# Kernel optimization log

Measured on AMD Instinct MI355X. Metric: run time of the kernel, lower is better.

The kernel has to match this reference:

```python
import math
import jax, jax.numpy as jnp
import numpy as np

# dims: batch, in-channels, out-channels, features (freq bins), frames, heads, expansion
B, C, CO, F, W, NH, EXP = 1, 8, 8, 512, 256, 8, 4
CC = C + CO          # channels into cross-attn query (cat of h and self_attn)
FC = C + 2 * CO      # channels into FFN (cat of h, self_attn, src_attn)
FH = F * EXP         # FFN hidden features


def mc_linear(x, pw, dw=None):
    # x: [B,Cin,Fin,W]; pw: [Cin,Fout,Fin] per-channel positionwise matmul;
    # dw: [Cout,Cin] channel-mixing matmul ('depthwise' in the repo's naming)
    y = jnp.einsum('bcfw,cgf->bcgw', x, pw)
    if dw is not None:
        y = jnp.einsum('bcgw,oc->bogw', y, dw)
    return y


def frame_conv(x, w, b):
    # Conv2d kernel (1,3), padding (0,1): 1D conv along the frame axis
    y = jax.lax.conv_general_dilated(x, w, (1, 1), ((0, 0), (1, 1)),
                                     dimension_numbers=('NCHW', 'OIHW', 'NCHW'))
    return y + b[None, :, None, None]


def mc_layernorm(x, g, b, eps=1e-5):
    # normalize over the feature axis (2), per (batch, channel, frame)
    mu = x.mean(axis=2, keepdims=True)
    var = jnp.mean(jnp.square(x - mu), axis=2, keepdims=True)
    return (x - mu) * jax.lax.rsqrt(var + eps) * g[None, :, :, None] + b[None, :, :, None]


def mc_attention(xq, xkv, q_pw, q_dw, q_cw, q_cb, k_pw, k_cw, k_cb, v_pw, v_cw, v_cb, o_pw):
    q = frame_conv(mc_linear(xq, q_pw, q_dw), q_cw, q_cb)   # [B,CO,F,Wq]
    k = frame_conv(mc_linear(xkv, k_pw), k_cw, k_cb)        # [B,CO,F,Wk]
    v = frame_conv(mc_linear(xkv, v_pw), v_cw, v_cb)
    dh = F // NH

    def heads(t):  # [B,CO,F,Wt] -> [B,CO,NH,Wt,dh]
        b_, c_, f_, w_ = t.shape
        return t.transpose(0, 1, 3, 2).reshape(b_, c_, w_, NH, dh).transpose(0, 1, 3, 2, 4)

    qh, kh, vh = heads(q), heads(k), heads(v)
    qk = jnp.einsum('bchqd,bchkd->bchqk', qh, kh) / math.sqrt(F)
    a = jnp.einsum('bchqk,bchkd->bchqd', jax.nn.softmax(qk, axis=-1), vh)
    b_, c_, h_, w_, _ = a.shape
    a = a.transpose(0, 1, 3, 2, 4).reshape(b_, c_, w_, F).transpose(0, 1, 3, 2)  # [B,CO,F,Wq]
    return mc_linear(a, o_pw), qk


def setup_inputs() -> dict:
    key = jax.random.key(0)
    ks = jax.random.split(key, 32)
    it = iter(range(32))

    def rn(shape, s=0.02):
        return jax.random.normal(ks[next(it)], shape, jnp.float32) * s

    inp = {
        'x': jax.random.normal(ks[next(it)], (B, C, F, W), jnp.float32),
        'src': jax.random.normal(ks[next(it)], (B, C, F, W), jnp.float32),
        'ln_g': jnp.ones((C, F), jnp.float32),
        'ln_b': jnp.zeros((C, F), jnp.float32),
        # self-attention (C -> CO, C == CO so no channel-mix on projections)
        'sa_q_pw': rn((C, F, F)), 'sa_q_cw': rn((CO, CO, 1, 3), 0.1), 'sa_q_cb': jnp.zeros((CO,), jnp.float32),
        'sa_k_pw': rn((C, F, F)), 'sa_k_cw': rn((CO, CO, 1, 3), 0.1), 'sa_k_cb': jnp.zeros((CO,), jnp.float32),
        'sa_v_pw': rn((C, F, F)), 'sa_v_cw': rn((CO, CO, 1, 3), 0.1), 'sa_v_cb': jnp.zeros((CO,), jnp.float32),
        'sa_o_pw': rn((CO, F, F)),
        # cross-attention (query from CC=C+CO channels -> CO; key/value from src with C channels)
        'ca_q_pw': rn((CC, F, F)), 'ca_q_dw': rn((CO, CC), 0.1),
        'ca_q_cw': rn((CO, CO, 1, 3), 0.1), 'ca_q_cb': jnp.zeros((CO,), jnp.float32),
        'ca_k_pw': rn((C, F, F)), 'ca_k_cw': rn((CO, CO, 1, 3), 0.1), 'ca_k_cb': jnp.zeros((CO,), jnp.float32),
        'ca_v_pw': rn((C, F, F)), 'ca_v_cw': rn((CO, CO, 1, 3), 0.1), 'ca_v_cb': jnp.zeros((CO,), jnp.float32),
        'ca_o_pw': rn((CO, F, F)),
        # FFN
        'ffn1_pw': rn((FC, FH, F)), 'ffn1_dw': rn((FC, FC), 0.1),
        'ffn2_pw': rn((FC, F, FH)), 'ffn2_dw': rn((C, FC), 0.1),
    }
    return inp


def reference(x, src, ln_g, ln_b,
              sa_q_pw, sa_q_cw, sa_q_cb, sa_k_pw, sa_k_cw, sa_k_cb, sa_v_pw, sa_v_cw, sa_v_cb, sa_o_pw,
              ca_q_pw, ca_q_dw, ca_q_cw, ca_q_cb, ca_k_pw, ca_k_cw, ca_k_cb, ca_v_pw, ca_v_cw, ca_v_cb, ca_o_pw,
              ffn1_pw, ffn1_dw, ffn2_pw, ffn2_dw):
    h = mc_layernorm(x, ln_g, ln_b)
    sa, qk1 = mc_attention(h, h, sa_q_pw, None, sa_q_cw, sa_q_cb,
                           sa_k_pw, sa_k_cw, sa_k_cb, sa_v_pw, sa_v_cw, sa_v_cb, sa_o_pw)
    ca, qk2 = mc_attention(jnp.concatenate([h, sa], axis=1), src,
                           ca_q_pw, ca_q_dw, ca_q_cw, ca_q_cb,
                           ca_k_pw, ca_k_cw, ca_k_cb, ca_v_pw, ca_v_cw, ca_v_cb, ca_o_pw)
    z = mc_linear(jnp.concatenate([h, sa, ca], axis=1), ffn1_pw, ffn1_dw)
    z = jax.nn.gelu(z, approximate=False)
    z = mc_linear(z, ffn2_pw, ffn2_dw)
    return (x + z, qk1, qk2)
```

## Files before the change

kernel.cpp:

```cpp
#include <hip/hip_runtime.h>
#include <math.h>

typedef __attribute__((ext_vector_type(4))) float f32x4;
typedef __attribute__((ext_vector_type(8))) short s16x8;
typedef __attribute__((ext_vector_type(4))) short s16x4;

__device__ __forceinline__ unsigned short f2b(float f) {
    union { float f; unsigned u; } v; v.f = f;
    unsigned r = v.u + 0x7fffu + ((v.u >> 16) & 1u);
    return (unsigned short)(r >> 16);
}
__device__ __forceinline__ float b2f(unsigned short u) {
    union { unsigned u; float f; } v; v.u = ((unsigned)u) << 16;
    return v.f;
}

__device__ __forceinline__ void gll16(const void* g, void* l) {
    __builtin_amdgcn_global_load_lds((const __attribute__((address_space(1))) unsigned int*)g,
                                     (__attribute__((address_space(3))) unsigned int*)l,
                                     16, 0, 0);
}

constexpr int kF = 512;
constexpr int kW = 256;
constexpr int kFW = kF * kW;

__global__ __launch_bounds__(256) void prep_kernel(const float* __restrict__ x,
                                                   const float* __restrict__ g,
                                                   const float* __restrict__ b,
                                                   unsigned short* __restrict__ hTb,
                                                   const float* __restrict__ src,
                                                   unsigned short* __restrict__ SRCT) {
    __shared__ float tile[64][65];
    __shared__ float s1[16][16], s2[16][16];
    int bid = blockIdx.x;
    int t = threadIdx.x;
    if (bid < 128) {
        int c = bid >> 4;
        int w0 = (bid & 15) * 16;
        int wi = t & 15, fg = t >> 4;
        const float* xb = x + (size_t)c * kFW + w0 + wi;
        float sum = 0.f, sum2 = 0.f;
        for (int j = 0; j < 32; ++j) {
            float v = xb[(size_t)(fg * 32 + j) * kW];
            sum += v; sum2 += v * v;
        }
        s1[fg][wi] = sum; s2[fg][wi] = sum2;
        __syncthreads();
        float ts = 0.f, tq = 0.f;
        #pragma unroll
        for (int j = 0; j < 16; ++j) { ts += s1[j][wi]; tq += s2[j][wi]; }
        float mu = ts * (1.0f / 512.0f);
        float rstd = rsqrtf(tq * (1.0f / 512.0f) - mu * mu + 1e-5f);
        const float* gc = g + c * kF + fg * 32;
        const float* bc = b + c * kF + fg * 32;
        unsigned short* ob = hTb + (size_t)c * kFW + (size_t)(w0 + wi) * kF + fg * 32;
        for (int j = 0; j < 32; j += 4) {
            float v0 = xb[(size_t)(fg * 32 + j + 0) * kW];
            float v1 = xb[(size_t)(fg * 32 + j + 1) * kW];
            float v2 = xb[(size_t)(fg * 32 + j + 2) * kW];
            float v3 = xb[(size_t)(fg * 32 + j + 3) * kW];
            s16x4 p = { (short)f2b((v0 - mu) * rstd * gc[j + 0] + bc[j + 0]),
                        (short)f2b((v1 - mu) * rstd * gc[j + 1] + bc[j + 1]),
                        (short)f2b((v2 - mu) * rstd * gc[j + 2] + bc[j + 2]),
                        (short)f2b((v3 - mu) * rstd * gc[j + 3] + bc[j + 3]) };
            *(s16x4*)(&ob[j]) = p;
        }
    } else {
        int fid = bid - 128;
        int c = fid >> 5;
        int f0 = ((fid >> 2) & 7) * 64, w0 = (fid & 3) * 64;
        int tw = t & 63, tf4 = t >> 6;
        for (int i = 0; i < 16; ++i) {
            int f = tf4 * 16 + i;
            tile[f][tw] = src[(size_t)c * kFW + (size_t)(f0 + f) * kW + w0 + tw];
        }
        __syncthreads();
        int w = t >> 2, fc = (t & 3) * 16;
        unsigned short* ob = SRCT + (size_t)c * kFW + (size_t)(w0 + w) * kF + f0 + fc;
        for (int j = 0; j < 16; j += 4) {
            s16x4 p = { (short)f2b(tile[fc + j + 0][w]), (short)f2b(tile[fc + j + 1][w]),
                        (short)f2b(tile[fc + j + 2][w]), (short)f2b(tile[fc + j + 3][w]) };
            *(s16x4*)(&ob[j]) = p;
        }
    }
}

struct WSeg { const float* A; const unsigned short* B; void* C; int omode; };
struct WB8 { WSeg s[8]; };

__global__ __launch_bounds__(256) void wgemm256(WB8 wb, int M, int K, int Klocal,
                                                long a_ch, long b_ch, long c_ch, long c_split,
                                                int segshift, int nm, int ksplit) {
    __shared__ unsigned short lds[16384];
    int t = threadIdx.x, lane = t & 63, wv = t >> 6;
    int l16 = lane & 15, l4 = lane >> 4;

    int id = blockIdx.x;
    int r = id & 7, j = id >> 3;
    int per = nm * ksplit;
    int y = r + 8 * (j / per);
    int rem = j % per;
    int mt = rem % nm;
    int kz = rem / nm;
    int seg = y >> segshift, c = y & ((1 << segshift) - 1);
    WSeg sg = wb.s[seg];
    int bm = mt * 64;
    int kbase = kz * Klocal;

    const float* A = sg.A + (size_t)c * a_ch + kbase;
    const unsigned short* Bc = sg.B + (size_t)c * b_ch + kbase;
    const float* arow = A + (size_t)(bm + wv * 16 + l16) * K + l4 * 8;

    int rsub = lane >> 3;
    int gsw = ((lane & 7) ^ rsub) * 8;
    const unsigned short* bsrc = Bc + (size_t)rsub * K + gsw;

    f32x4 acc[16];
    #pragma unroll
    for (int i = 0; i < 16; ++i) acc[i] = (f32x4){0.f, 0.f, 0.f, 0.f};

    f32x4 pa0 = __builtin_nontemporal_load((const f32x4*)arow);
    f32x4 pa1 = __builtin_nontemporal_load((const f32x4*)(arow + 4));

    for (int kc = 0; kc < Klocal; kc += 64) {
        if (kc) __syncthreads();
        #pragma unroll
        for (int i = 0; i < 8; ++i) {
            int r0 = wv * 64 + i * 8;
            gll16(bsrc + (size_t)r0 * K + kc, (char*)lds + (r0 << 7));
        }
        __syncthreads();
        #pragma unroll
        for (int ks = 0; ks < 2; ++ks) {
            f32x4 c0 = pa0, c1 = pa1;
            int nk = kc + (ks + 1) * 32;
            if (nk < Klocal) {
                pa0 = __builtin_nontemporal_load((const f32x4*)(arow + nk));
                pa1 = __builtin_nontemporal_load((const f32x4*)(arow + nk + 4));
            }
            s16x8 af = { (short)f2b(c0.x), (short)f2b(c0.y), (short)f2b(c0.z), (short)f2b(c0.w),
                         (short)f2b(c1.x), (short)f2b(c1.y), (short)f2b(c1.z), (short)f2b(c1.w) };
            #pragma unroll
            for (int ni = 0; ni < 16; ++ni) {
                int rr = ni * 16 + l16;
                s16x8 bf = *(const s16x8*)(&lds[rr * 64 + ((ks * 32 + l4 * 8) ^ ((rr & 7) << 3))]);
                acc[ni] = __builtin_amdgcn_mfma_f32_16x16x32_bf16(af, bf, acc[ni], 0, 0, 0);
            }
        }
    }

    int m0 = bm + wv * 16 + l4 * 4;
    if (sg.omode == 2) {
        unsigned short* C = (unsigned short*)sg.C + (size_t)c * c_ch;
        #pragma unroll
        for (int ni = 0; ni < 16; ++ni) {
            int n = ni * 16 + l16;
            s16x4 pk = { (short)f2b(acc[ni][0]), (short)f2b(acc[ni][1]),
                         (short)f2b(acc[ni][2]), (short)f2b(acc[ni][3]) };
            *(s16x4*)(&C[(size_t)n * M + m0]) = pk;
        }
    } else if (sg.omode == 1) {
        unsigned short* C = (unsigned short*)sg.C + (size_t)c * c_ch;
        #pragma unroll
        for (int ni = 0; ni < 16; ++ni) {
            int n = ni * 16 + l16;
            #pragma unroll
            for (int rr = 0; rr < 4; ++rr)
                C[(size_t)(m0 + rr) * 256 + n] = f2b(acc[ni][rr]);
        }
    } else {
        float* C = (float*)sg.C + (size_t)c * c_ch + (size_t)kz * c_split;
        #pragma unroll
        for (int ni = 0; ni < 16; ++ni) {
            int n = ni * 16 + l16;
            #pragma unroll
            for (int rr = 0; rr < 4; ++rr)
                C[(size_t)(m0 + rr) * 256 + n] = acc[ni][rr];
        }
    }
}

__global__ __launch_bounds__(256) void attn_kernel(
    const unsigned short* __restrict__ Qt, const unsigned short* __restrict__ Kt,
    const unsigned short* __restrict__ VN, float* __restrict__ S,
    unsigned short* __restrict__ ATTT, float scale)
{
    __shared__ unsigned short q_lds[4096];
    __shared__ unsigned short kv_lds[16384];
    __shared__ unsigned short p_lds[16384];
    __shared__ float smax[4][64], ssum[4][64], sinv[64];
    int t = threadIdx.x, lane = t & 63, wv = t >> 6;
    int l16 = lane & 15, l4 = lane >> 4;
    int ch = blockIdx.y, c = ch >> 3, h = ch & 7;
    int bm = blockIdx.x * 64;
    const unsigned short* Qb = Qt + (size_t)c * kFW + h * 64;
    const unsigned short* Kb = Kt + (size_t)c * kFW + h * 64;
    const unsigned short* Vb = VN + (size_t)c * kFW + (size_t)(h * 64) * 256;
    float* Sb = S + (size_t)ch * 65536;
    unsigned short* Ab = ATTT + (size_t)c * kFW + h * 64;

    s16x8 qr[2], kr[8], vr[8];
    #pragma unroll
    for (int i = 0; i < 2; ++i) {
        int idx = i * 256 + t; int rr = idx >> 3, ck = idx & 7;
        qr[i] = *(const s16x8*)(Qb + (size_t)(bm + rr) * 512 + ck * 8);
    }
    #pragma unroll
    for (int i = 0; i < 8; ++i) {
        int idx = i * 256 + t; int rr = idx >> 3, ck = idx & 7;
        kr[i] = *(const s16x8*)(Kb + (size_t)rr * 512 + ck * 8);
    }
    #pragma unroll
    for (int i = 0; i < 8; ++i) {
        int idx = i * 256 + t; int d = idx >> 5, cs = idx & 31;
        vr[i] = *(const s16x8*)(Vb + (size_t)d * 256 + cs * 8);
    }
    #pragma unroll
    for (int i = 0; i < 2; ++i) {
        int idx = i * 256 + t; int rr = idx >> 3, ck = idx & 7;
        *(s16x8*)(&q_lds[rr * 64 + ((ck * 8) ^ ((rr & 7) << 3))]) = qr[i];
    }
    #pragma unroll
    for (int i = 0; i < 8; ++i) {
        int idx = i * 256 + t; int rr = idx >> 3, ck = idx & 7;
        *(s16x8*)(&kv_lds[rr * 64 + ((ck * 8) ^ ((rr & 7) << 3))]) = kr[i];
    }
    __syncthreads();

    f32x4 acc[4][4];
    #pragma unroll
    for (int i = 0; i < 4; ++i)
        #pragma unroll
        for (int jj = 0; jj < 4; ++jj) acc[i][jj] = (f32x4){0.f, 0.f, 0.f, 0.f};
    #pragma unroll
    for (int ks = 0; ks < 2; ++ks) {
        s16x8 af[4], bfr[4];
        #pragma unroll
        for (int mi = 0; mi < 4; ++mi) {
            int rq = mi * 16 + l16;
            af[mi] = *(const s16x8*)(&q_lds[rq * 64 + ((ks * 32 + l4 * 8) ^ ((rq & 7) << 3))]);
        }
        #pragma unroll
        for (int ni = 0; ni < 4; ++ni) {
            int rk = wv * 64 + ni * 16 + l16;
            bfr[ni] = *(const s16x8*)(&kv_lds[rk * 64 + ((ks * 32 + l4 * 8) ^ ((rk & 7) << 3))]);
        }
        #pragma unroll
        for (int mi = 0; mi < 4; ++mi)
            #pragma unroll
            for (int ni = 0; ni < 4; ++ni)
                acc[mi][ni] = __builtin_amdgcn_mfma_f32_16x16x32_bf16(af[mi], bfr[ni], acc[mi][ni], 0, 0, 0);
    }

    #pragma unroll
    for (int mi = 0; mi < 4; ++mi)
        #pragma unroll
        for (int ni = 0; ni < 4; ++ni) {
            acc[mi][ni] *= scale;
            int col = wv * 64 + ni * 16 + l16;
            int row0 = bm + mi * 16 + l4 * 4;
            #pragma unroll
            for (int rr = 0; rr < 4; ++rr)
                Sb[(size_t)(row0 + rr) * 256 + col] = acc[mi][ni][rr];
        }

    float rmax[4][4];
    #pragma unroll
    for (int mi = 0; mi < 4; ++mi)
        #pragma unroll
        for (int rr = 0; rr < 4; ++rr)
            rmax[mi][rr] = fmaxf(fmaxf(acc[mi][0][rr], acc[mi][1][rr]), fmaxf(acc[mi][2][rr], acc[mi][3][rr]));
    #pragma unroll
    for (int d = 1; d < 16; d <<= 1)
        #pragma unroll
        for (int mi = 0; mi < 4; ++mi)
            #pragma unroll
            for (int rr = 0; rr < 4; ++rr)
                rmax[mi][rr] = fmaxf(rmax[mi][rr], __shfl_xor(rmax[mi][rr], d));
    if (l16 == 0)
        #pragma unroll
        for (int mi = 0; mi < 4; ++mi)
            #pragma unroll
            for (int rr = 0; rr < 4; ++rr)
                smax[wv][mi * 16 + l4 * 4 + rr] = rmax[mi][rr];
    __syncthreads();
    float rsum[4][4];
    #pragma unroll
    for (int mi = 0; mi < 4; ++mi)
        #pragma unroll
        for (int rr = 0; rr < 4; ++rr) {
            int row = mi * 16 + l4 * 4 + rr;
            float rM = fmaxf(fmaxf(smax[0][row], smax[1][row]), fmaxf(smax[2][row], smax[3][row]));
            rsum[mi][rr] = 0.f;
            #pragma unroll
            for (int ni = 0; ni < 4; ++ni) {
                float e = __expf(acc[mi][ni][rr] - rM);
                acc[mi][ni][rr] = e;
                rsum[mi][rr] += e;
            }
        }
    #pragma unroll
    for (int d = 1; d < 16; d <<= 1)
        #pragma unroll
        for (int mi = 0; mi < 4; ++mi)
            #pragma unroll
            for (int rr = 0; rr < 4; ++rr)
                rsum[mi][rr] += __shfl_xor(rsum[mi][rr], d);
    if (l16 == 0)
        #pragma unroll
        for (int mi = 0; mi < 4; ++mi)
            #pragma unroll
            for (int rr = 0; rr < 4; ++rr)
                ssum[wv][mi * 16 + l4 * 4 + rr] = rsum[mi][rr];
    __syncthreads();

    #pragma unroll
    for (int i = 0; i < 8; ++i) {
        int idx = i * 256 + t; int d = idx >> 5, cs = idx & 31;
        *(s16x8*)(&kv_lds[d * 256 + ((cs * 8) ^ ((d & 7) << 3))]) = vr[i];
    }
    #pragma unroll
    for (int mi = 0; mi < 4; ++mi)
        #pragma unroll
        for (int ni = 0; ni < 4; ++ni) {
            int col = wv * 64 + ni * 16 + l16;
            int cb = col & ~7, cl = col & 7;
            #pragma unroll
            for (int rr = 0; rr < 4; ++rr) {
                int row = mi * 16 + l4 * 4 + rr;
                p_lds[row * 256 + (cb ^ ((row & 7) << 3)) + cl] = f2b(acc[mi][ni][rr]);
            }
        }
    if (t < 64) sinv[t] = 1.f / (ssum[0][t] + ssum[1][t] + ssum[2][t] + ssum[3][t]);
    __syncthreads();

    f32x4 po[4];
    #pragma unroll
    for (int ni = 0; ni < 4; ++ni) po[ni] = (f32x4){0.f, 0.f, 0.f, 0.f};
    int qrow = wv * 16 + l16;
    #pragma unroll
    for (int ks = 0; ks < 8; ++ks) {
        s16x8 paf = *(const s16x8*)(&p_lds[qrow * 256 + ((ks * 32 + l4 * 8) ^ ((qrow & 7) << 3))]);
        #pragma unroll
        for (int ni = 0; ni < 4; ++ni) {
            int rd = ni * 16 + l16;
            s16x8 bf = *(const s16x8*)(&kv_lds[rd * 256 + ((ks * 32 + l4 * 8) ^ ((rd & 7) << 3))]);
            po[ni] = __builtin_amdgcn_mfma_f32_16x16x32_bf16(paf, bf, po[ni], 0, 0, 0);
        }
    }
    #pragma unroll
    for (int ni = 0; ni < 4; ++ni) {
        int d = ni * 16 + l16;
        #pragma unroll
        for (int rr = 0; rr < 4; ++rr) {
            int row = wv * 16 + l4 * 4 + rr;
            Ab[(size_t)(bm + row) * 512 + d] = f2b(po[ni][rr] * sinv[row]);
        }
    }
}

struct ConvArgs {
    const unsigned short* in[5];
    unsigned short* out[5];
    const float* cw[5];
    const float* cb[5];
    int mode[5];
};

__global__ __launch_bounds__(256) void conv5_kernel(ConvArgs a) {
    int g = blockIdx.y;
    __shared__ float scw[192]; __shared__ float scb[8];
    int t = threadIdx.x;
    if (t < 192) scw[t] = a.cw[g][t];
    if (t >= 192 && t < 200) scb[t - 192] = a.cb[g][t - 192];
    __syncthreads();
    const unsigned short* in = a.in[g];
    unsigned short* out = a.out[g];
    int gi = blockIdx.x * 256 + t;
    int mode = a.mode[g];
    int w = mode ? (gi & 255) : (gi >> 9);
    int str = mode ? 1 : 512;
    float acc[8];
    #pragma unroll
    for (int o = 0; o < 8; ++o) acc[o] = scb[o];
    bool hm = w > 0, hp = w < 255;
    #pragma unroll
    for (int i = 0; i < 8; ++i) {
        size_t base = (size_t)i * kFW + gi;
        float xm = hm ? b2f(in[base - str]) : 0.f;
        float x0 = b2f(in[base]);
        float xp = hp ? b2f(in[base + str]) : 0.f;
        #pragma unroll
        for (int o = 0; o < 8; ++o) {
            const float* wp = &scw[(o * 8 + i) * 3];
            acc[o] += wp[0] * xm + wp[1] * x0 + wp[2] * xp;
        }
    }
    #pragma unroll
    for (int o = 0; o < 8; ++o) out[(size_t)o * kFW + gi] = f2b(acc[o]);
}

__global__ __launch_bounds__(256) void mixconv_kernel(const unsigned short* __restrict__ in,
                                                      const float* __restrict__ dw,
                                                      const float* __restrict__ cw,
                                                      const float* __restrict__ cb,
                                                      unsigned short* __restrict__ out) {
    __shared__ float sdw[128], scw[192], scb[8];
    int t = threadIdx.x;
    if (t < 128) sdw[t] = dw[t];
    if (t >= 128 && t < 136) scb[t - 128] = cb[t - 128];
    if (t < 192) scw[t] = cw[t];
    __syncthreads();
    int gi = blockIdx.x * 256 + t;
    int w = gi >> 9;
    bool hm = w > 0, hp = w < 255;
    float xc[16], xm[16], xp[16];
    #pragma unroll
    for (int cc = 0; cc < 16; ++cc) {
        size_t base = (size_t)cc * kFW + gi;
        xc[cc] = b2f(in[base]);
        xm[cc] = hm ? b2f(in[base - 512]) : 0.f;
        xp[cc] = hp ? b2f(in[base + 512]) : 0.f;
    }
    float mm[8], m0[8], mp[8];
    #pragma unroll
    for (int o = 0; o < 8; ++o) {
        float am = 0.f, a0 = 0.f, ap = 0.f;
        #pragma unroll
        for (int cc = 0; cc < 16; ++cc) {
            float wv = sdw[o * 16 + cc];
            am += wv * xm[cc]; a0 += wv * xc[cc]; ap += wv * xp[cc];
        }
        mm[o] = am; m0[o] = a0; mp[o] = ap;
    }
    #pragma unroll
    for (int o = 0; o < 8; ++o) {
        float acc = scb[o];
        #pragma unroll
        for (int i = 0; i < 8; ++i) {
            const float* wp = &scw[(o * 8 + i) * 3];
            acc += wp[0] * mm[i] + wp[1] * m0[i] + wp[2] * mp[i];
        }
        out[(size_t)o * kFW + gi] = f2b(acc);
    }
}

__global__ __launch_bounds__(256) void gelu24_kernel(unsigned short* __restrict__ z,
                                                     const float* __restrict__ dw) {
    __shared__ float sdw[576];
    int t = threadIdx.x;
    for (int i = t; i < 576; i += 256) sdw[i] = dw[i];
    __syncthreads();
    size_t gi = (size_t)blockIdx.x * 256 + t;
    const size_t CH = (size_t)256 * 2048;
    float xv[24];
    #pragma unroll
    for (int cc = 0; cc < 24; ++cc) xv[cc] = b2f(z[cc * CH + gi]);
    #pragma unroll
    for (int o = 0; o < 24; ++o) {
        float s = 0.f;
        #pragma unroll
        for (int cc = 0; cc < 24; ++cc) s += sdw[o * 24 + cc] * xv[cc];
        s = 0.5f * s * (1.0f + erff(s * 0.7071067811865475f));
        z[o * CH + gi] = f2b(s);
    }
}

__global__ __launch_bounds__(256) void final_mix_add2(const float* __restrict__ x,
                                                      const float* __restrict__ z2,
                                                      const float* __restrict__ dw,
                                                      float* __restrict__ out) {
    __shared__ float sdw[192];
    int t = threadIdx.x;
    if (t < 192) sdw[t] = dw[t];
    __syncthreads();
    int gi = blockIdx.x * 256 + t;
    const size_t PSZ = (size_t)24 * kFW;
    float xv[24];
    #pragma unroll
    for (int cc = 0; cc < 24; ++cc) {
        size_t o = (size_t)cc * kFW + gi;
        xv[cc] = z2[o] + z2[PSZ + o];
    }
    #pragma unroll
    for (int o = 0; o < 8; ++o) {
        float s = 0.f;
        #pragma unroll
        for (int cc = 0; cc < 24; ++cc) s += sdw[o * 24 + cc] * xv[cc];
        out[(size_t)o * kFW + gi] = x[(size_t)o * kFW + gi] + s;
    }
}

extern "C" void kernel_launch(void* const* d_in, const int* in_sizes, int n_in,
                              void* d_out, int out_size, void* d_ws, size_t ws_size,
                              hipStream_t stream) {
    const float* x       = (const float*)d_in[0];
    const float* src     = (const float*)d_in[1];
    const float* ln_g    = (const float*)d_in[2];
    const float* ln_b    = (const float*)d_in[3];
    const float* sa_q_pw = (const float*)d_in[4];
    const float* sa_q_cw = (const float*)d_in[5];
    const float* sa_q_cb = (const float*)d_in[6];
    const float* sa_k_pw = (const float*)d_in[7];
    const float* sa_k_cw = (const float*)d_in[8];
    const float* sa_k_cb = (const float*)d_in[9];
    const float* sa_v_pw = (const float*)d_in[10];
    const float* sa_v_cw = (const float*)d_in[11];
    const float* sa_v_cb = (const float*)d_in[12];
    const float* sa_o_pw = (const float*)d_in[13];
    const float* ca_q_pw = (const float*)d_in[14];
    const float* ca_q_dw = (const float*)d_in[15];
    const float* ca_q_cw = (const float*)d_in[16];
    const float* ca_q_cb = (const float*)d_in[17];
    const float* ca_k_pw = (const float*)d_in[18];
    const float* ca_k_cw = (const float*)d_in[19];
    const float* ca_k_cb = (const float*)d_in[20];
    const float* ca_v_pw = (const float*)d_in[21];
    const float* ca_v_cw = (const float*)d_in[22];
    const float* ca_v_cb = (const float*)d_in[23];
    const float* ca_o_pw = (const float*)d_in[24];
    const float* ffn1_pw = (const float*)d_in[25];
    const float* ffn1_dw = (const float*)d_in[26];
    const float* ffn2_pw = (const float*)d_in[27];
    const float* ffn2_dw = (const float*)d_in[28];

    float* out  = (float*)d_out;
    float* qk1o = out + 1048576;
    float* qk2o = out + 1048576 + 4194304;

    unsigned char* ws = (unsigned char*)d_ws;
    unsigned short* CAT24  = (unsigned short*)(ws + 0);
    unsigned short* hTb    = CAT24;
    unsigned short* saTb   = CAT24 + 8 * (size_t)kFW;
    unsigned short* caTb   = CAT24 + 16 * (size_t)kFW;
    unsigned short* SRCT   = (unsigned short*)(ws + 6291456);
    unsigned short* preQ   = (unsigned short*)(ws + 8388608);
    unsigned short* preK   = (unsigned short*)(ws + 10485760);
    unsigned short* preVsa = (unsigned short*)(ws + 12582912);
    unsigned short* preKca = (unsigned short*)(ws + 14680064);
    unsigned short* preVca = (unsigned short*)(ws + 16777216);
    unsigned short* QT     = (unsigned short*)(ws + 18874368);
    unsigned short* KT     = (unsigned short*)(ws + 20971520);
    unsigned short* VNsa   = (unsigned short*)(ws + 23068672);
    unsigned short* KTca   = (unsigned short*)(ws + 25165824);
    unsigned short* VNca   = (unsigned short*)(ws + 27262976);
    unsigned short* PRE16  = (unsigned short*)(ws + 29360128);
    unsigned short* QTca   = (unsigned short*)(ws + 33554432);
    unsigned short* ATTT   = (unsigned short*)(ws + 35651584);
    unsigned short* Z0T    = (unsigned short*)(ws + 8388608);
    float*          Z2P    = (float*)(ws + 37748736);

    const float qscale = 0.044194173824159216f;
    dim3 blk(256);

    prep_kernel<<<384, blk, 0, stream>>>(x, ln_g, ln_b, hTb, src, SRCT);

    WB8 p6;
    p6.s[0] = { sa_q_pw, hTb,  preQ,   2 };
    p6.s[1] = { sa_k_pw, hTb,  preK,   2 };
    p6.s[2] = { sa_v_pw, hTb,  preVsa, 1 };
    p6.s[3] = { ca_k_pw, SRCT, preKca, 2 };
    p6.s[4] = { ca_v_pw, SRCT, preVca, 1 };
    p6.s[5] = { ca_q_pw, hTb,  PRE16,  2 };
    p6.s[6] = p6.s[0]; p6.s[7] = p6.s[0];
    wgemm256<<<dim3(384), blk, 0, stream>>>(p6, 512, 512, 512, 262144, kFW, kFW, 0, 3, 8, 1);

    ConvArgs c5;
    c5.in[0] = preQ;   c5.out[0] = QT;   c5.cw[0] = sa_q_cw; c5.cb[0] = sa_q_cb; c5.mode[0] = 0;
    c5.in[1] = preK;   c5.out[1] = KT;   c5.cw[1] = sa_k_cw; c5.cb[1] = sa_k_cb; c5.mode[1] = 0;
    c5.in[2] = preVsa; c5.out[2] = VNsa; c5.cw[2] = sa_v_cw; c5.cb[2] = sa_v_cb; c5.mode[2] = 1;
    c5.in[3] = preKca; c5.out[3] = KTca; c5.cw[3] = ca_k_cw; c5.cb[3] = ca_k_cb; c5.mode[3] = 0;
    c5.in[4] = preVca; c5.out[4] = VNca; c5.cw[4] = ca_v_cw; c5.cb[4] = ca_v_cb; c5.mode[4] = 1;
    conv5_kernel<<<dim3(512, 5), blk, 0, stream>>>(c5);

    attn_kernel<<<dim3(4, 64), blk, 0, stream>>>(QT, KT, VNsa, qk1o, ATTT, qscale);
    WB8 so;
    so.s[0] = { sa_o_pw, ATTT, saTb, 2 };
    for (int i = 1; i < 8; ++i) so.s[i] = so.s[0];
    wgemm256<<<dim3(64), blk, 0, stream>>>(so, 512, 512, 512, 262144, kFW, kFW, 0, 8, 8, 1);

    WB8 cq2;
    cq2.s[0] = { ca_q_pw + 8 * 262144, saTb, PRE16 + 8 * (size_t)kFW, 2 };
    for (int i = 1; i < 8; ++i) cq2.s[i] = cq2.s[0];
    wgemm256<<<dim3(64), blk, 0, stream>>>(cq2, 512, 512, 512, 262144, kFW, kFW, 0, 8, 8, 1);
    mixconv_kernel<<<512, blk, 0, stream>>>(PRE16, ca_q_dw, ca_q_cw, ca_q_cb, QTca);

    attn_kernel<<<dim3(4, 64), blk, 0, stream>>>(QTca, KTca, VNca, qk2o, ATTT, qscale);
    WB8 co;
    co.s[0] = { ca_o_pw, ATTT, caTb, 2 };
    for (int i = 1; i < 8; ++i) co.s[i] = co.s[0];
    wgemm256<<<dim3(64), blk, 0, stream>>>(co, 512, 512, 512, 262144, kFW, kFW, 0, 8, 8, 1);

    WB8 f1;
    f1.s[0] = { ffn1_pw, CAT24, Z0T, 2 };
    for (int i = 1; i < 8; ++i) f1.s[i] = f1.s[0];
    wgemm256<<<dim3(768), blk, 0, stream>>>(f1, 2048, 512, 512, 1048576, kFW, 524288, 0, 8, 32, 1);
    gelu24_kernel<<<2048, blk, 0, stream>>>(Z0T, ffn1_dw);
    WB8 f2;
    f2.s[0] = { ffn2_pw, Z0T, Z2P, 0 };
    for (int i = 1; i < 8; ++i) f2.s[i] = f2.s[0];
    wgemm256<<<dim3(384), blk, 0, stream>>>(f2, 512, 2048, 1024, 1048576, 524288, kFW, 3145728, 8, 8, 2);
    final_mix_add2<<<512, blk, 0, stream>>>(x, Z2P, ffn2_dw, out);
}
```

Baseline: 271.7 us.

## Use 512-thread GEMM blocks with 128-row tiles and double-buffered B in LDS

The batched per-channel GEMM now runs 8 waves per block covering 128 output rows, so each B tile staged in LDS is shared by twice as many rows. B loads are double-buffered, with the next 64-wide K chunk prefetched while MFMAs run on the current one, which removes one barrier per iteration. Grid sizes are halved to match. The cost is twice the LDS per block (64 KB) and fewer blocks, which may reduce occupancy and leave CUs idle on the small 32-block launches.

```diff
diff --git a/kernel.cpp b/kernel.cpp
--- a/kernel.cpp
+++ b/kernel.cpp
@@ -89,10 +89,10 @@
 struct WSeg { const float* A; const unsigned short* B; void* C; int omode; };
 struct WB8 { WSeg s[8]; };
 
-__global__ __launch_bounds__(256) void wgemm256(WB8 wb, int M, int K, int Klocal,
+__global__ __launch_bounds__(512) void wgemm512(WB8 wb, int M, int K, int Klocal,
                                                 long a_ch, long b_ch, long c_ch, long c_split,
                                                 int segshift, int nm, int ksplit) {
-    __shared__ unsigned short lds[16384];
+    __shared__ unsigned short lds[2][16384];
     int t = threadIdx.x, lane = t & 63, wv = t >> 6;
     int l16 = lane & 15, l4 = lane >> 4;
 
@@ -105,7 +105,7 @@
     int kz = rem / nm;
     int seg = y >> segshift, c = y & ((1 << segshift) - 1);
     WSeg sg = wb.s[seg];
-    int bm = mt * 64;
+    int bm = mt * 128;
     int kbase = kz * Klocal;
 
     const float* A = sg.A + (size_t)c * a_ch + kbase;
@@ -114,27 +114,34 @@
 
     int rsub = lane >> 3;
     int gsw = ((lane & 7) ^ rsub) * 8;
-    const unsigned short* bsrc = Bc + (size_t)rsub * K + gsw;
+    const unsigned short* bsrc = Bc + (size_t)(wv * 32 + rsub) * K + gsw;
 
     f32x4 acc[16];
     #pragma unroll
     for (int i = 0; i < 16; ++i) acc[i] = (f32x4){0.f, 0.f, 0.f, 0.f};
+
+    #pragma unroll
+    for (int i = 0; i < 4; ++i)
+        gll16(bsrc + (size_t)(i * 8) * K, (char*)lds[0] + ((wv * 32 + i * 8) << 7));
 
     f32x4 pa0 = __builtin_nontemporal_load((const f32x4*)arow);
     f32x4 pa1 = __builtin_nontemporal_load((const f32x4*)(arow + 4));
 
-    for (int kc = 0; kc < Klocal; kc += 64) {
-        if (kc) __syncthreads();
-        #pragma unroll
-        for (int i = 0; i < 8; ++i) {
-            int r0 = wv * 64 + i * 8;
-            gll16(bsrc + (size_t)r0 * K + kc, (char*)lds + (r0 << 7));
-        }
+    int nc = Klocal >> 6;
+    for (int cc = 0; cc < nc; ++cc) {
         __syncthreads();
+        if (cc + 1 < nc) {
+            int kc = (cc + 1) * 64;
+            #pragma unroll
+            for (int i = 0; i < 4; ++i)
+                gll16(bsrc + (size_t)(i * 8) * K + kc,
+                      (char*)lds[(cc + 1) & 1] + ((wv * 32 + i * 8) << 7));
+        }
+        const unsigned short* buf = lds[cc & 1];
         #pragma unroll
         for (int ks = 0; ks < 2; ++ks) {
             f32x4 c0 = pa0, c1 = pa1;
-            int nk = kc + (ks + 1) * 32;
+            int nk = cc * 64 + (ks + 1) * 32;
             if (nk < Klocal) {
                 pa0 = __builtin_nontemporal_load((const f32x4*)(arow + nk));
                 pa1 = __builtin_nontemporal_load((const f32x4*)(arow + nk + 4));
@@ -144,7 +151,7 @@
             #pragma unroll
             for (int ni = 0; ni < 16; ++ni) {
                 int rr = ni * 16 + l16;
-                s16x8 bf = *(const s16x8*)(&lds[rr * 64 + ((ks * 32 + l4 * 8) ^ ((rr & 7) << 3))]);
+                s16x8 bf = *(const s16x8*)(&buf[rr * 64 + ((ks * 32 + l4 * 8) ^ ((rr & 7) << 3))]);
                 acc[ni] = __builtin_amdgcn_mfma_f32_16x16x32_bf16(af, bf, acc[ni], 0, 0, 0);
             }
         }
@@ -553,6 +560,7 @@
 
     const float qscale = 0.044194173824159216f;
     dim3 blk(256);
+    dim3 blk512(512);
 
     prep_kernel<<<384, blk, 0, stream>>>(x, ln_g, ln_b, hTb, src, SRCT);
 
@@ -564,7 +572,7 @@
     p6.s[4] = { ca_v_pw, SRCT, preVca, 1 };
     p6.s[5] = { ca_q_pw, hTb,  PRE16,  2 };
     p6.s[6] = p6.s[0]; p6.s[7] = p6.s[0];
-    wgemm256<<<dim3(384), blk, 0, stream>>>(p6, 512, 512, 512, 262144, kFW, kFW, 0, 3, 8, 1);
+    wgemm512<<<dim3(192), blk512, 0, stream>>>(p6, 512, 512, 512, 262144, kFW, kFW, 0, 3, 4, 1);
 
     ConvArgs c5;
     c5.in[0] = preQ;   c5.out[0] = QT;   c5.cw[0] = sa_q_cw; c5.cb[0] = sa_q_cb; c5.mode[0] = 0;
@@ -578,28 +586,28 @@
     WB8 so;
     so.s[0] = { sa_o_pw, ATTT, saTb, 2 };
     for (int i = 1; i < 8; ++i) so.s[i] = so.s[0];
-    wgemm256<<<dim3(64), blk, 0, stream>>>(so, 512, 512, 512, 262144, kFW, kFW, 0, 8, 8, 1);
+    wgemm512<<<dim3(32), blk512, 0, stream>>>(so, 512, 512, 512, 262144, kFW, kFW, 0, 8, 4, 1);
 
     WB8 cq2;
     cq2.s[0] = { ca_q_pw + 8 * 262144, saTb, PRE16 + 8 * (size_t)kFW, 2 };
     for (int i = 1; i < 8; ++i) cq2.s[i] = cq2.s[0];
-    wgemm256<<<dim3(64), blk, 0, stream>>>(cq2, 512, 512, 512, 262144, kFW, kFW, 0, 8, 8, 1);
+    wgemm512<<<dim3(32), blk512, 0, stream>>>(cq2, 512, 512, 512, 262144, kFW, kFW, 0, 8, 4, 1);
     mixconv_kernel<<<512, blk, 0, stream>>>(PRE16, ca_q_dw, ca_q_cw, ca_q_cb, QTca);
 
     attn_kernel<<<dim3(4, 64), blk, 0, stream>>>(QTca, KTca, VNca, qk2o, ATTT, qscale);
     WB8 co;
     co.s[0] = { ca_o_pw, ATTT, caTb, 2 };
     for (int i = 1; i < 8; ++i) co.s[i] = co.s[0];
-    wgemm256<<<dim3(64), blk, 0, stream>>>(co, 512, 512, 512, 262144, kFW, kFW, 0, 8, 8, 1);
+    wgemm512<<<dim3(32), blk512, 0, stream>>>(co, 512, 512, 512, 262144, kFW, kFW, 0, 8, 4, 1);
 
     WB8 f1;
     f1.s[0] = { ffn1_pw, CAT24, Z0T, 2 };
     for (int i = 1; i < 8; ++i) f1.s[i] = f1.s[0];
-    wgemm256<<<dim3(768), blk, 0, stream>>>(f1, 2048, 512, 512, 1048576, kFW, 524288, 0, 8, 32, 1);
+    wgemm512<<<dim3(384), blk512, 0, stream>>>(f1, 2048, 512, 512, 1048576, kFW, 524288, 0, 8, 16, 1);
     gelu24_kernel<<<2048, blk, 0, stream>>>(Z0T, ffn1_dw);
     WB8 f2;
     f2.s[0] = { ffn2_pw, Z0T, Z2P, 0 };
     for (int i = 1; i < 8; ++i) f2.s[i] = f2.s[0];
-    wgemm256<<<dim3(384), blk, 0, stream>>>(f2, 512, 2048, 1024, 1048576, 524288, kFW, 3145728, 8, 8, 2);
+    wgemm512<<<dim3(192), blk512, 0, stream>>>(f2, 512, 2048, 1024, 1048576, 524288, kFW, 3145728, 8, 4, 2);
     final_mix_add2<<<512, blk, 0, stream>>>(x, Z2P, ffn2_dw, out);
 }
```

New measurement: 285.9 us. 5.2% more time.
